# Optimization experiments

Measured on AMD Instinct MI355X. Metric: run time of the kernel, lower is better.

## Reference

```python
import jax, jax.numpy as jnp
import numpy as np

N_NODES = 100000
N_EDGES = 1000000
D_MODEL = 128
EDGE_DIM = 64
LN_EPS = 1e-5


def _layernorm(x, gamma, beta, eps=LN_EPS):
    mu = jnp.mean(x, axis=-1, keepdims=True)
    var = jnp.var(x, axis=-1, keepdims=True)
    return (x - mu) * jax.lax.rsqrt(var + eps) * gamma + beta


def setup_inputs() -> dict:
    key = jax.random.key(0)
    ks = jax.random.split(key, 12)
    std = 1.0 / np.sqrt(D_MODEL)
    stde = 1.0 / np.sqrt(EDGE_DIM)
    return {
        "x_src": jax.random.normal(ks[0], (N_NODES, D_MODEL), jnp.float32),
        "x_dst": jax.random.normal(ks[1], (N_NODES, D_MODEL), jnp.float32),
        "edge_attr": jax.random.normal(ks[2], (N_EDGES, EDGE_DIM), jnp.float32),
        "edge_index": jax.random.randint(ks[3], (2, N_EDGES), 0, N_NODES, jnp.int32),
        # params
        "W_src": jax.random.uniform(ks[4], (D_MODEL, D_MODEL), jnp.float32, -std, std),
        "W_dst": jax.random.uniform(ks[5], (D_MODEL, D_MODEL), jnp.float32, -std, std),
        "b_dst": jnp.zeros((D_MODEL,), jnp.float32),
        "Wg1": jax.random.uniform(ks[6], (EDGE_DIM, D_MODEL), jnp.float32, -stde, stde),
        "bg1": jnp.zeros((D_MODEL,), jnp.float32),
        "Wg2": jax.random.uniform(ks[7], (D_MODEL, 1), jnp.float32, -std, std),
        "bg2": jnp.zeros((1,), jnp.float32),
        "gamma": jnp.ones((D_MODEL,), jnp.float32),
        "beta": jnp.zeros((D_MODEL,), jnp.float32),
    }


def reference(x_src, x_dst, edge_attr, edge_index,
              W_src, W_dst, b_dst, Wg1, bg1, Wg2, bg2, gamma, beta):
    s, d = edge_index[0], edge_index[1]
    n = x_dst.shape[0]
    # gather + linear (no bias): [E, D]
    msg = x_src[s] @ W_src
    # edge gate MLP: Linear -> gelu -> Linear (no norm, eval so no dropout)
    h = jax.nn.gelu(edge_attr @ Wg1 + bg1, approximate=False)
    gate = jax.nn.sigmoid(h @ Wg2 + bg2)  # [E, 1]
    msg = msg * gate
    # scatter-add aggregate + mean by in-degree (clamped at 1)
    out = jax.ops.segment_sum(msg, d, num_segments=n)
    deg = jax.ops.segment_sum(jnp.ones((msg.shape[0],), msg.dtype), d, num_segments=n)
    out = out / jnp.clip(deg, 1.0)[:, None]
    # residual-like combine, layernorm, gelu
    out = _layernorm(out + x_dst @ W_dst + b_dst, gamma, beta)
    return jax.nn.gelu(out, approximate=False)
```

## Files before the change

kernel.cpp:

```cpp
#include <hip/hip_runtime.h>
#include <hip/hip_fp16.h>
#include <math.h>

#define N_NODES 100000
#define N_EDGES 1000000
#define D_MODEL 128
#define EDGE_DIM 64
#define SCHUNK 250
#define NSB 400

typedef short bf16x8 __attribute__((ext_vector_type(8)));
typedef float f32x4 __attribute__((ext_vector_type(4)));

__device__ __forceinline__ short f2bf(float f) {
    union { float f; unsigned u; } v; v.f = f;
    unsigned r = v.u + 0x7FFFu + ((v.u >> 16) & 1u);
    return (short)(r >> 16);
}
__device__ __forceinline__ float gelu_fast(float x) {
    float t = 0.7978845608028654f * x * (1.0f + 0.044715f * x * x);
    float e = __expf(2.0f * t);
    return x * (1.0f - __builtin_amdgcn_rcpf(e + 1.0f));
}
__device__ __forceinline__ float sigmoid_fast(float x) {
    return __builtin_amdgcn_rcpf(1.0f + __expf(-x));
}
__device__ __forceinline__ float bflo(unsigned v) { return __uint_as_float(v << 16); }
__device__ __forceinline__ float bfhi(unsigned v) { return __uint_as_float(v & 0xFFFF0000u); }

__global__ __launch_bounds__(256) void k_zero_int(int* __restrict__ p, int n) {
    int i = blockIdx.x * 256 + threadIdx.x;
    if (i < n) p[i] = 0;
}

__global__ __launch_bounds__(256) void k_prep(
    const float* __restrict__ Ws, const float* __restrict__ Wd,
    const float* __restrict__ Wg1, short* __restrict__ frag)
{
    int g = blockIdx.x * 256 + threadIdx.x;
    if (g >= 5120) return;
    const float* W; short* T; int q;
    if (g < 2048)      { W = Ws;  T = frag;         q = g; }
    else if (g < 4096) { W = Wd;  T = frag + 16384; q = g - 2048; }
    else               { W = Wg1; T = frag + 32768; q = g - 4096; }
    int ls = q & 63, nt = (q >> 6) & 7, kb = q >> 9;
    int col = nt * 16 + (ls & 15);
    int k0 = kb * 32 + (ls >> 4) * 8;
    bf16x8 v;
    #pragma unroll
    for (int e = 0; e < 8; ++e) v[e] = f2bf(W[(k0 + e) * D_MODEL + col]);
    *reinterpret_cast<bf16x8*>(T + (size_t)q * 8) = v;
}

__global__ __launch_bounds__(256, 2) void k_node_linear(
    const float* __restrict__ x_src, const float* __restrict__ x_dst,
    const short* __restrict__ WsrcF, const short* __restrict__ WdstF,
    const float* __restrict__ b_dst,
    short* __restrict__ ysrc, short* __restrict__ z_bf)
{
    __shared__ __align__(16) short Bf[4][8][64][8];
    const int tid = threadIdx.x;
    const int lane = tid & 63;
    const int wid = tid >> 6;
    const int l15 = lane & 15;
    const int lg = lane >> 4;
    const int mat = blockIdx.y;
    const float* __restrict__ X = mat ? x_dst : x_src;
    const short* __restrict__ WF = mat ? WdstF : WsrcF;
    const int row0 = blockIdx.x * 128 + wid * 32;

    float4 av[4][2][2];
    #pragma unroll
    for (int kb = 0; kb < 4; ++kb)
        #pragma unroll
        for (int st = 0; st < 2; ++st) {
            int r = min(row0 + st * 16 + l15, N_NODES - 1);
            const float* p = X + (size_t)r * D_MODEL + kb * 32 + lg * 8;
            av[kb][st][0] = *reinterpret_cast<const float4*>(p);
            av[kb][st][1] = *reinterpret_cast<const float4*>(p + 4);
        }
    #pragma unroll
    for (int i = 0; i < 8; ++i)
        reinterpret_cast<int4*>(Bf)[tid + i * 256] =
            reinterpret_cast<const int4*>(WF)[tid + i * 256];
    __syncthreads();

    bf16x8 a[4][2];
    #pragma unroll
    for (int kb = 0; kb < 4; ++kb)
        #pragma unroll
        for (int st = 0; st < 2; ++st) {
            float4 v0 = av[kb][st][0], v1 = av[kb][st][1];
            bf16x8 t;
            t[0] = f2bf(v0.x); t[1] = f2bf(v0.y); t[2] = f2bf(v0.z); t[3] = f2bf(v0.w);
            t[4] = f2bf(v1.x); t[5] = f2bf(v1.y); t[6] = f2bf(v1.z); t[7] = f2bf(v1.w);
            a[kb][st] = t;
        }

    f32x4 acc[2][8];
    #pragma unroll
    for (int st = 0; st < 2; ++st)
        #pragma unroll
        for (int nt = 0; nt < 8; ++nt) { f32x4 zz = {0.f,0.f,0.f,0.f}; acc[st][nt] = zz; }

    #pragma unroll
    for (int kb = 0; kb < 4; ++kb)
        #pragma unroll
        for (int nt = 0; nt < 8; ++nt) {
            bf16x8 b = *reinterpret_cast<const bf16x8*>(&Bf[kb][nt][lane][0]);
            acc[0][nt] = __builtin_amdgcn_mfma_f32_16x16x32_bf16(a[kb][0], b, acc[0][nt], 0, 0, 0);
            acc[1][nt] = __builtin_amdgcn_mfma_f32_16x16x32_bf16(a[kb][1], b, acc[1][nt], 0, 0, 0);
        }

    #pragma unroll
    for (int st = 0; st < 2; ++st) {
        int rowb = row0 + st * 16 + lg * 4;
        #pragma unroll
        for (int nt = 0; nt < 8; ++nt) {
            int col = nt * 16 + l15;
            float bias = mat ? b_dst[col] : 0.0f;
            #pragma unroll
            for (int r = 0; r < 4; ++r) {
                int row = rowb + r;
                if (row < N_NODES) {
                    float v = acc[st][nt][r];
                    if (mat) z_bf[(size_t)row * D_MODEL + col] = f2bf(v + bias);
                    else     ysrc[(size_t)row * D_MODEL + col] = f2bf(v);
                }
            }
        }
    }
}

__global__ __launch_bounds__(256, 4) void k_gate_fill(
    const float* __restrict__ ea, const short* __restrict__ Wg1F,
    const float* __restrict__ bg1, const float* __restrict__ Wg2,
    const float* __restrict__ bg2,
    const int* __restrict__ dstI, const int* __restrict__ srcI,
    int* __restrict__ cursor, int* __restrict__ sg_s,
    unsigned short* __restrict__ sg_g)
{
    __shared__ __align__(16) short Bf[2][8][64][8];
    const int tid = threadIdx.x;
    const int lane = tid & 63;
    const int wid = tid >> 6;
    const int l15 = lane & 15;
    const int lg = lane >> 4;
    const int e0 = blockIdx.x * 128 + wid * 32;

    float4 av[2][2][2];
    #pragma unroll
    for (int kb = 0; kb < 2; ++kb)
        #pragma unroll
        for (int st = 0; st < 2; ++st) {
            int r = min(e0 + st * 16 + l15, N_EDGES - 1);
            const float* p = ea + (size_t)r * EDGE_DIM + kb * 32 + lg * 8;
            av[kb][st][0] = *reinterpret_cast<const float4*>(p);
            av[kb][st][1] = *reinterpret_cast<const float4*>(p + 4);
        }
    float b1v[2][4], w2v[2][4];
    #pragma unroll
    for (int ntc = 0; ntc < 2; ++ntc)
        #pragma unroll
        for (int nt = 0; nt < 4; ++nt) {
            int col = (ntc * 4 + nt) * 16 + l15;
            b1v[ntc][nt] = bg1[col];
            w2v[ntc][nt] = Wg2[col];
        }
    #pragma unroll
    for (int i = 0; i < 4; ++i)
        reinterpret_cast<int4*>(Bf)[tid + i * 256] =
            reinterpret_cast<const int4*>(Wg1F)[tid + i * 256];
    __syncthreads();

    bf16x8 a[2][2];
    #pragma unroll
    for (int kb = 0; kb < 2; ++kb)
        #pragma unroll
        for (int st = 0; st < 2; ++st) {
            float4 v0 = av[kb][st][0], v1 = av[kb][st][1];
            bf16x8 t;
            t[0] = f2bf(v0.x); t[1] = f2bf(v0.y); t[2] = f2bf(v0.z); t[3] = f2bf(v0.w);
            t[4] = f2bf(v1.x); t[5] = f2bf(v1.y); t[6] = f2bf(v1.z); t[7] = f2bf(v1.w);
            a[kb][st] = t;
        }

    float part[2][4] = {{0.f,0.f,0.f,0.f},{0.f,0.f,0.f,0.f}};
    #pragma unroll
    for (int ntc = 0; ntc < 2; ++ntc) {
        f32x4 acc[2][4];
        #pragma unroll
        for (int st = 0; st < 2; ++st)
            #pragma unroll
            for (int nt = 0; nt < 4; ++nt) { f32x4 zz = {0.f,0.f,0.f,0.f}; acc[st][nt] = zz; }
        #pragma unroll
        for (int kb = 0; kb < 2; ++kb)
            #pragma unroll
            for (int nt = 0; nt < 4; ++nt) {
                bf16x8 b = *reinterpret_cast<const bf16x8*>(&Bf[kb][ntc * 4 + nt][lane][0]);
                acc[0][nt] = __builtin_amdgcn_mfma_f32_16x16x32_bf16(a[kb][0], b, acc[0][nt], 0, 0, 0);
                acc[1][nt] = __builtin_amdgcn_mfma_f32_16x16x32_bf16(a[kb][1], b, acc[1][nt], 0, 0, 0);
            }
        #pragma unroll
        for (int nt = 0; nt < 4; ++nt) {
            float b1 = b1v[ntc][nt], w2 = w2v[ntc][nt];
            #pragma unroll
            for (int st = 0; st < 2; ++st)
                #pragma unroll
                for (int r = 0; r < 4; ++r)
                    part[st][r] += gelu_fast(acc[st][nt][r] + b1) * w2;
        }
    }

    #pragma unroll
    for (int m = 1; m <= 8; m <<= 1)
        #pragma unroll
        for (int st = 0; st < 2; ++st)
            #pragma unroll
            for (int r = 0; r < 4; ++r)
                part[st][r] += __shfl_xor(part[st][r], m);

    if (l15 == 0) {
        float b2 = bg2[0];
        #pragma unroll
        for (int st = 0; st < 2; ++st)
            #pragma unroll
            for (int r = 0; r < 4; ++r) {
                int e = e0 + st * 16 + lg * 4 + r;
                if (e < N_EDGES) {
                    float gv = sigmoid_fast(part[st][r] + b2);
                    int d = dstI[e];
                    int s = srcI[e];
                    int p = atomicAdd(&cursor[d], 1);
                    __half h = __float2half(gv);
                    sg_s[p] = s;
                    sg_g[p] = *reinterpret_cast<unsigned short*>(&h);
                }
            }
    }
}

__global__ void k_deg(const int* __restrict__ dst, int* __restrict__ deg) {
    int e = blockIdx.x * 256 + threadIdx.x;
    if (e < N_EDGES) atomicAdd(&deg[dst[e]], 1);
}
__global__ __launch_bounds__(256) void k_scan1(const int* __restrict__ deg, int* __restrict__ bsum) {
    __shared__ int s[256];
    int tid = threadIdx.x;
    int i = blockIdx.x * SCHUNK + tid;
    int v = (tid < SCHUNK && i < N_NODES) ? deg[i] : 0;
    s[tid] = v; __syncthreads();
    for (int off = 128; off > 0; off >>= 1) {
        if (tid < off) s[tid] += s[tid + off];
        __syncthreads();
    }
    if (tid == 0) bsum[blockIdx.x] = s[0];
}
__global__ __launch_bounds__(512) void k_scan2(const int* __restrict__ bsum, int* __restrict__ boff) {
    __shared__ int s[512];
    int tid = threadIdx.x;
    int v = (tid < NSB) ? bsum[tid] : 0;
    s[tid] = v; __syncthreads();
    for (int off = 1; off < 512; off <<= 1) {
        int t = (tid >= off) ? s[tid - off] : 0;
        __syncthreads();
        s[tid] += t;
        __syncthreads();
    }
    if (tid < NSB) boff[tid] = s[tid] - v;
}
__global__ __launch_bounds__(256) void k_scan3(const int* __restrict__ deg, const int* __restrict__ boff,
                                               int* __restrict__ cursor) {
    __shared__ int s[256];
    int tid = threadIdx.x;
    int i = blockIdx.x * SCHUNK + tid;
    int v = (tid < SCHUNK && i < N_NODES) ? deg[i] : 0;
    s[tid] = v; __syncthreads();
    for (int off = 1; off < 256; off <<= 1) {
        int t = (tid >= off) ? s[tid - off] : 0;
        __syncthreads();
        s[tid] += t;
        __syncthreads();
    }
    int excl = s[tid] - v;
    if (tid < SCHUNK && i < N_NODES) cursor[i] = boff[blockIdx.x] + excl;
}

__global__ __launch_bounds__(256) void k_agg(
    const int* __restrict__ cursorEnd, const int* __restrict__ deg,
    const int* __restrict__ sg_s, const __half* __restrict__ sg_g,
    const short* __restrict__ ysrc, const short* __restrict__ z_bf,
    const float* __restrict__ gamma, const float* __restrict__ beta,
    float* __restrict__ out)
{
    const int lane = threadIdx.x & 63;
    const int wid = threadIdx.x >> 6;
    const int n = blockIdx.x * 4 + wid;
    const int dg = deg[n];
    const int start = cursorEnd[n] - dg;
    const int c0 = lane * 2;

    float a0 = 0.f, a1 = 0.f;
    int t = 0;
    for (; t + 4 <= dg; t += 4) {
        int s0 = sg_s[start + t + 0];
        int s1 = sg_s[start + t + 1];
        int s2 = sg_s[start + t + 2];
        int s3 = sg_s[start + t + 3];
        float g0 = __half2float(sg_g[start + t + 0]);
        float g1 = __half2float(sg_g[start + t + 1]);
        float g2 = __half2float(sg_g[start + t + 2]);
        float g3 = __half2float(sg_g[start + t + 3]);
        unsigned p0 = *reinterpret_cast<const unsigned*>(&ysrc[(size_t)s0 * D_MODEL + c0]);
        unsigned p1 = *reinterpret_cast<const unsigned*>(&ysrc[(size_t)s1 * D_MODEL + c0]);
        unsigned p2 = *reinterpret_cast<const unsigned*>(&ysrc[(size_t)s2 * D_MODEL + c0]);
        unsigned p3 = *reinterpret_cast<const unsigned*>(&ysrc[(size_t)s3 * D_MODEL + c0]);
        a0 += g0 * bflo(p0) + g1 * bflo(p1) + g2 * bflo(p2) + g3 * bflo(p3);
        a1 += g0 * bfhi(p0) + g1 * bfhi(p1) + g2 * bfhi(p2) + g3 * bfhi(p3);
    }
    for (; t < dg; ++t) {
        int s0 = sg_s[start + t];
        float g0 = __half2float(sg_g[start + t]);
        unsigned p0 = *reinterpret_cast<const unsigned*>(&ysrc[(size_t)s0 * D_MODEL + c0]);
        a0 += g0 * bflo(p0);
        a1 += g0 * bfhi(p0);
    }

    float inv = 1.0f / fmaxf((float)dg, 1.0f);
    unsigned zv = *reinterpret_cast<const unsigned*>(&z_bf[(size_t)n * D_MODEL + c0]);
    float t0 = a0 * inv + bflo(zv);
    float t1 = a1 * inv + bfhi(zv);

    float sum = t0 + t1;
    #pragma unroll
    for (int m = 1; m <= 32; m <<= 1) sum += __shfl_xor(sum, m);
    float mu = sum * (1.0f / 128.0f);
    float d0 = t0 - mu, d1 = t1 - mu;
    float vs = d0 * d0 + d1 * d1;
    #pragma unroll
    for (int m = 1; m <= 32; m <<= 1) vs += __shfl_xor(vs, m);
    float rstd = rsqrtf(vs * (1.0f / 128.0f) + 1e-5f);

    float2 gv = *reinterpret_cast<const float2*>(&gamma[c0]);
    float2 bv = *reinterpret_cast<const float2*>(&beta[c0]);
    float o0 = d0 * rstd * gv.x + bv.x;
    float o1 = d1 * rstd * gv.y + bv.y;
    float2 o = make_float2(gelu_fast(o0), gelu_fast(o1));
    *reinterpret_cast<float2*>(&out[(size_t)n * D_MODEL + c0]) = o;
}

extern "C" void kernel_launch(void* const* d_in, const int* in_sizes, int n_in,
                              void* d_out, int out_size, void* d_ws, size_t ws_size,
                              hipStream_t stream)
{
    const float* x_src = (const float*)d_in[0];
    const float* x_dst = (const float*)d_in[1];
    const float* ea    = (const float*)d_in[2];
    const int*   ei    = (const int*)d_in[3];
    const float* W_src = (const float*)d_in[4];
    const float* W_dst = (const float*)d_in[5];
    const float* b_dst = (const float*)d_in[6];
    const float* Wg1   = (const float*)d_in[7];
    const float* bg1   = (const float*)d_in[8];
    const float* Wg2   = (const float*)d_in[9];
    const float* bg2   = (const float*)d_in[10];
    const float* gamma = (const float*)d_in[11];
    const float* beta  = (const float*)d_in[12];
    const int* srcIdx = ei;
    const int* dstIdx = ei + N_EDGES;

    char* ws = (char*)d_ws;
    short*  fragT  = (short*)(ws);
    short*  ysrc   = (short*)(ws + 81920);
    short*  z_bf   = (short*)(ws + 25681920);
    int*    deg    = (int*)(ws + 51281920);
    int*    cursor = (int*)(ws + 51681920);
    int*    sg_s   = (int*)(ws + 52081920);
    unsigned short* sg_g = (unsigned short*)(ws + 56081920);
    int*    bsum   = (int*)(ws + 58081920);
    int*    boff   = (int*)(ws + 58083520);

    float* out = (float*)d_out;

    hipLaunchKernelGGL(k_zero_int, dim3((N_NODES + 255) / 256), dim3(256), 0, stream, deg, N_NODES);
    hipLaunchKernelGGL(k_deg, dim3(3907), dim3(256), 0, stream, dstIdx, deg);
    hipLaunchKernelGGL(k_scan1, dim3(NSB), dim3(256), 0, stream, deg, bsum);
    hipLaunchKernelGGL(k_scan2, dim3(1), dim3(512), 0, stream, bsum, boff);
    hipLaunchKernelGGL(k_scan3, dim3(NSB), dim3(256), 0, stream, deg, boff, cursor);
    hipLaunchKernelGGL(k_prep, dim3(20), dim3(256), 0, stream, W_src, W_dst, Wg1, fragT);
    hipLaunchKernelGGL(k_node_linear, dim3(782, 2), dim3(256), 0, stream,
                       x_src, x_dst, fragT, fragT + 16384, b_dst, ysrc, z_bf);
    hipLaunchKernelGGL(k_gate_fill, dim3(7813), dim3(256), 0, stream,
                       ea, fragT + 32768, bg1, Wg2, bg2, dstIdx, srcIdx, cursor, sg_s, sg_g);
    hipLaunchKernelGGL(k_agg, dim3(N_NODES / 4), dim3(256), 0, stream,
                       cursor, deg, sg_s, (const __half*)sg_g, ysrc, z_bf, gamma, beta, out);
}
```

Measured before the change: 293.5 us.

## Record per-edge rank in degree pass, pack CSR entries, fuse zeroing into prep

The degree-count atomic now returns each edge's rank, so the gate kernel computes its CSR slot directly from rstart[d] + rank[e] and no longer needs a second atomic on a cursor array. Source index and gate are packed into one int2 entry (the gate stays fp32 instead of fp16), so the aggregation reads a single 8-byte record per edge and gets its node range from rstart[n], rstart[n+1]. Degree zeroing is merged into the weight-prep kernel, removing one launch. Node-linear gains a double-buffered row load and a higher occupancy hint, and gate-fill loads its bias and weights inside the loop instead of holding them in registers. The cost is an extra 4 MB rank array that must be written and read back, plus larger CSR entries.

```diff
diff --git a/kernel.cpp b/kernel.cpp
--- a/kernel.cpp
+++ b/kernel.cpp
@@ -28,16 +28,18 @@
 __device__ __forceinline__ float bflo(unsigned v) { return __uint_as_float(v << 16); }
 __device__ __forceinline__ float bfhi(unsigned v) { return __uint_as_float(v & 0xFFFF0000u); }
 
-__global__ __launch_bounds__(256) void k_zero_int(int* __restrict__ p, int n) {
-    int i = blockIdx.x * 256 + threadIdx.x;
-    if (i < n) p[i] = 0;
-}
-
 __global__ __launch_bounds__(256) void k_prep(
     const float* __restrict__ Ws, const float* __restrict__ Wd,
-    const float* __restrict__ Wg1, short* __restrict__ frag)
+    const float* __restrict__ Wg1, short* __restrict__ frag,
+    int* __restrict__ deg)
 {
-    int g = blockIdx.x * 256 + threadIdx.x;
+    int b = blockIdx.x;
+    if (b >= 20) {
+        int i = (b - 20) * 256 + threadIdx.x;
+        if (i < N_NODES) deg[i] = 0;
+        return;
+    }
+    int g = b * 256 + threadIdx.x;
     if (g >= 5120) return;
     const float* W; short* T; int q;
     if (g < 2048)      { W = Ws;  T = frag;         q = g; }
@@ -52,7 +54,57 @@
     *reinterpret_cast<bf16x8*>(T + (size_t)q * 8) = v;
 }
 
-__global__ __launch_bounds__(256, 2) void k_node_linear(
+__global__ void k_deg(const int* __restrict__ dst, int* __restrict__ deg, int* __restrict__ rank) {
+    int e = blockIdx.x * 256 + threadIdx.x;
+    if (e < N_EDGES) rank[e] = atomicAdd(&deg[dst[e]], 1);
+}
+
+__global__ __launch_bounds__(256) void k_scan1(const int* __restrict__ deg, int* __restrict__ bsum) {
+    __shared__ int s[256];
+    int tid = threadIdx.x;
+    int i = blockIdx.x * SCHUNK + tid;
+    int v = (tid < SCHUNK && i < N_NODES) ? deg[i] : 0;
+    s[tid] = v; __syncthreads();
+    for (int off = 128; off > 0; off >>= 1) {
+        if (tid < off) s[tid] += s[tid + off];
+        __syncthreads();
+    }
+    if (tid == 0) bsum[blockIdx.x] = s[0];
+}
+__global__ __launch_bounds__(512) void k_scan2(const int* __restrict__ bsum, int* __restrict__ boff) {
+    __shared__ int s[512];
+    int tid = threadIdx.x;
+    int v = (tid < NSB) ? bsum[tid] : 0;
+    s[tid] = v; __syncthreads();
+    for (int off = 1; off < 512; off <<= 1) {
+        int t = (tid >= off) ? s[tid - off] : 0;
+        __syncthreads();
+        s[tid] += t;
+        __syncthreads();
+    }
+    if (tid < NSB) boff[tid] = s[tid] - v;
+}
+__global__ __launch_bounds__(256) void k_scan3(const int* __restrict__ deg, const int* __restrict__ boff,
+                                               int* __restrict__ rstart) {
+    __shared__ int s[256];
+    int tid = threadIdx.x;
+    int i = blockIdx.x * SCHUNK + tid;
+    int v = (tid < SCHUNK && i < N_NODES) ? deg[i] : 0;
+    s[tid] = v; __syncthreads();
+    for (int off = 1; off < 256; off <<= 1) {
+        int t = (tid >= off) ? s[tid - off] : 0;
+        __syncthreads();
+        s[tid] += t;
+        __syncthreads();
+    }
+    int excl = s[tid] - v;
+    if (tid < SCHUNK && i < N_NODES) {
+        rstart[i] = boff[blockIdx.x] + excl;
+        if (i == N_NODES - 1) rstart[N_NODES] = boff[blockIdx.x] + excl + v;
+    }
+}
+
+__global__ __launch_bounds__(256, 3) void k_node_linear(
     const float* __restrict__ x_src, const float* __restrict__ x_dst,
     const short* __restrict__ WsrcF, const short* __restrict__ WdstF,
     const float* __restrict__ b_dst,
@@ -69,48 +121,58 @@
     const short* __restrict__ WF = mat ? WdstF : WsrcF;
     const int row0 = blockIdx.x * 128 + wid * 32;
 
-    float4 av[4][2][2];
-    #pragma unroll
-    for (int kb = 0; kb < 4; ++kb)
-        #pragma unroll
-        for (int st = 0; st < 2; ++st) {
-            int r = min(row0 + st * 16 + l15, N_NODES - 1);
-            const float* p = X + (size_t)r * D_MODEL + kb * 32 + lg * 8;
-            av[kb][st][0] = *reinterpret_cast<const float4*>(p);
-            av[kb][st][1] = *reinterpret_cast<const float4*>(p + 4);
-        }
+    const float* rowp[2];
+    #pragma unroll
+    for (int st = 0; st < 2; ++st) {
+        int r = min(row0 + st * 16 + l15, N_NODES - 1);
+        rowp[st] = X + (size_t)r * D_MODEL + lg * 8;
+    }
+
+    float4 buf[2][2][2];
+    #pragma unroll
+    for (int st = 0; st < 2; ++st) {
+        buf[0][st][0] = *reinterpret_cast<const float4*>(rowp[st]);
+        buf[0][st][1] = *reinterpret_cast<const float4*>(rowp[st] + 4);
+    }
+
     #pragma unroll
     for (int i = 0; i < 8; ++i)
         reinterpret_cast<int4*>(Bf)[tid + i * 256] =
             reinterpret_cast<const int4*>(WF)[tid + i * 256];
+
+    f32x4 acc[2][8];
+    #pragma unroll
+    for (int st = 0; st < 2; ++st)
+        #pragma unroll
+        for (int nt = 0; nt < 8; ++nt) { f32x4 zz = {0.f,0.f,0.f,0.f}; acc[st][nt] = zz; }
+
     __syncthreads();
 
-    bf16x8 a[4][2];
-    #pragma unroll
-    for (int kb = 0; kb < 4; ++kb)
+    #pragma unroll
+    for (int kb = 0; kb < 4; ++kb) {
+        if (kb < 3) {
+            #pragma unroll
+            for (int st = 0; st < 2; ++st) {
+                buf[(kb + 1) & 1][st][0] = *reinterpret_cast<const float4*>(rowp[st] + (kb + 1) * 32);
+                buf[(kb + 1) & 1][st][1] = *reinterpret_cast<const float4*>(rowp[st] + (kb + 1) * 32 + 4);
+            }
+        }
+        bf16x8 a[2];
         #pragma unroll
         for (int st = 0; st < 2; ++st) {
-            float4 v0 = av[kb][st][0], v1 = av[kb][st][1];
+            float4 v0 = buf[kb & 1][st][0], v1 = buf[kb & 1][st][1];
             bf16x8 t;
             t[0] = f2bf(v0.x); t[1] = f2bf(v0.y); t[2] = f2bf(v0.z); t[3] = f2bf(v0.w);
             t[4] = f2bf(v1.x); t[5] = f2bf(v1.y); t[6] = f2bf(v1.z); t[7] = f2bf(v1.w);
-            a[kb][st] = t;
-        }
-
-    f32x4 acc[2][8];
-    #pragma unroll
-    for (int st = 0; st < 2; ++st)
-        #pragma unroll
-        for (int nt = 0; nt < 8; ++nt) { f32x4 zz = {0.f,0.f,0.f,0.f}; acc[st][nt] = zz; }
-
-    #pragma unroll
-    for (int kb = 0; kb < 4; ++kb)
+            a[st] = t;
+        }
         #pragma unroll
         for (int nt = 0; nt < 8; ++nt) {
             bf16x8 b = *reinterpret_cast<const bf16x8*>(&Bf[kb][nt][lane][0]);
-            acc[0][nt] = __builtin_amdgcn_mfma_f32_16x16x32_bf16(a[kb][0], b, acc[0][nt], 0, 0, 0);
-            acc[1][nt] = __builtin_amdgcn_mfma_f32_16x16x32_bf16(a[kb][1], b, acc[1][nt], 0, 0, 0);
-        }
+            acc[0][nt] = __builtin_amdgcn_mfma_f32_16x16x32_bf16(a[0], b, acc[0][nt], 0, 0, 0);
+            acc[1][nt] = __builtin_amdgcn_mfma_f32_16x16x32_bf16(a[1], b, acc[1][nt], 0, 0, 0);
+        }
+    }
 
     #pragma unroll
     for (int st = 0; st < 2; ++st) {
@@ -137,8 +199,8 @@
     const float* __restrict__ bg1, const float* __restrict__ Wg2,
     const float* __restrict__ bg2,
     const int* __restrict__ dstI, const int* __restrict__ srcI,
-    int* __restrict__ cursor, int* __restrict__ sg_s,
-    unsigned short* __restrict__ sg_g)
+    const int* __restrict__ rank, const int* __restrict__ rstart,
+    int2* __restrict__ sg)
 {
     __shared__ __align__(16) short Bf[2][8][64][8];
     const int tid = threadIdx.x;
@@ -158,15 +220,6 @@
             av[kb][st][0] = *reinterpret_cast<const float4*>(p);
             av[kb][st][1] = *reinterpret_cast<const float4*>(p + 4);
         }
-    float b1v[2][4], w2v[2][4];
-    #pragma unroll
-    for (int ntc = 0; ntc < 2; ++ntc)
-        #pragma unroll
-        for (int nt = 0; nt < 4; ++nt) {
-            int col = (ntc * 4 + nt) * 16 + l15;
-            b1v[ntc][nt] = bg1[col];
-            w2v[ntc][nt] = Wg2[col];
-        }
     #pragma unroll
     for (int i = 0; i < 4; ++i)
         reinterpret_cast<int4*>(Bf)[tid + i * 256] =
@@ -203,7 +256,9 @@
             }
         #pragma unroll
         for (int nt = 0; nt < 4; ++nt) {
-            float b1 = b1v[ntc][nt], w2 = w2v[ntc][nt];
+            int col = (ntc * 4 + nt) * 16 + l15;
+            float b1 = bg1[col];
+            float w2 = Wg2[col];
             #pragma unroll
             for (int st = 0; st < 2; ++st)
                 #pragma unroll
@@ -230,65 +285,16 @@
                 if (e < N_EDGES) {
                     float gv = sigmoid_fast(part[st][r] + b2);
                     int d = dstI[e];
-                    int s = srcI[e];
-                    int p = atomicAdd(&cursor[d], 1);
-                    __half h = __float2half(gv);
-                    sg_s[p] = s;
-                    sg_g[p] = *reinterpret_cast<unsigned short*>(&h);
+                    int p = rstart[d] + rank[e];
+                    int2 v; v.x = srcI[e]; v.y = __float_as_int(gv);
+                    sg[p] = v;
                 }
             }
     }
 }
 
-__global__ void k_deg(const int* __restrict__ dst, int* __restrict__ deg) {
-    int e = blockIdx.x * 256 + threadIdx.x;
-    if (e < N_EDGES) atomicAdd(&deg[dst[e]], 1);
-}
-__global__ __launch_bounds__(256) void k_scan1(const int* __restrict__ deg, int* __restrict__ bsum) {
-    __shared__ int s[256];
-    int tid = threadIdx.x;
-    int i = blockIdx.x * SCHUNK + tid;
-    int v = (tid < SCHUNK && i < N_NODES) ? deg[i] : 0;
-    s[tid] = v; __syncthreads();
-    for (int off = 128; off > 0; off >>= 1) {
-        if (tid < off) s[tid] += s[tid + off];
-        __syncthreads();
-    }
-    if (tid == 0) bsum[blockIdx.x] = s[0];
-}
-__global__ __launch_bounds__(512) void k_scan2(const int* __restrict__ bsum, int* __restrict__ boff) {
-    __shared__ int s[512];
-    int tid = threadIdx.x;
-    int v = (tid < NSB) ? bsum[tid] : 0;
-    s[tid] = v; __syncthreads();
-    for (int off = 1; off < 512; off <<= 1) {
-        int t = (tid >= off) ? s[tid - off] : 0;
-        __syncthreads();
-        s[tid] += t;
-        __syncthreads();
-    }
-    if (tid < NSB) boff[tid] = s[tid] - v;
-}
-__global__ __launch_bounds__(256) void k_scan3(const int* __restrict__ deg, const int* __restrict__ boff,
-                                               int* __restrict__ cursor) {
-    __shared__ int s[256];
-    int tid = threadIdx.x;
-    int i = blockIdx.x * SCHUNK + tid;
-    int v = (tid < SCHUNK && i < N_NODES) ? deg[i] : 0;
-    s[tid] = v; __syncthreads();
-    for (int off = 1; off < 256; off <<= 1) {
-        int t = (tid >= off) ? s[tid - off] : 0;
-        __syncthreads();
-        s[tid] += t;
-        __syncthreads();
-    }
-    int excl = s[tid] - v;
-    if (tid < SCHUNK && i < N_NODES) cursor[i] = boff[blockIdx.x] + excl;
-}
-
 __global__ __launch_bounds__(256) void k_agg(
-    const int* __restrict__ cursorEnd, const int* __restrict__ deg,
-    const int* __restrict__ sg_s, const __half* __restrict__ sg_g,
+    const int* __restrict__ rstart, const int2* __restrict__ sg,
     const short* __restrict__ ysrc, const short* __restrict__ z_bf,
     const float* __restrict__ gamma, const float* __restrict__ beta,
     float* __restrict__ out)
@@ -296,38 +302,40 @@
     const int lane = threadIdx.x & 63;
     const int wid = threadIdx.x >> 6;
     const int n = blockIdx.x * 4 + wid;
-    const int dg = deg[n];
-    const int start = cursorEnd[n] - dg;
+    const int start = rstart[n];
+    const int end = rstart[n + 1];
+    const int dg = end - start;
     const int c0 = lane * 2;
 
+    unsigned zv = *reinterpret_cast<const unsigned*>(&z_bf[(size_t)n * D_MODEL + c0]);
+    float2 gv = *reinterpret_cast<const float2*>(&gamma[c0]);
+    float2 bv = *reinterpret_cast<const float2*>(&beta[c0]);
+
     float a0 = 0.f, a1 = 0.f;
-    int t = 0;
-    for (; t + 4 <= dg; t += 4) {
-        int s0 = sg_s[start + t + 0];
-        int s1 = sg_s[start + t + 1];
-        int s2 = sg_s[start + t + 2];
-        int s3 = sg_s[start + t + 3];
-        float g0 = __half2float(sg_g[start + t + 0]);
-        float g1 = __half2float(sg_g[start + t + 1]);
-        float g2 = __half2float(sg_g[start + t + 2]);
-        float g3 = __half2float(sg_g[start + t + 3]);
-        unsigned p0 = *reinterpret_cast<const unsigned*>(&ysrc[(size_t)s0 * D_MODEL + c0]);
-        unsigned p1 = *reinterpret_cast<const unsigned*>(&ysrc[(size_t)s1 * D_MODEL + c0]);
-        unsigned p2 = *reinterpret_cast<const unsigned*>(&ysrc[(size_t)s2 * D_MODEL + c0]);
-        unsigned p3 = *reinterpret_cast<const unsigned*>(&ysrc[(size_t)s3 * D_MODEL + c0]);
+    int t = start;
+    for (; t + 4 <= end; t += 4) {
+        int2 e0 = sg[t + 0];
+        int2 e1 = sg[t + 1];
+        int2 e2 = sg[t + 2];
+        int2 e3 = sg[t + 3];
+        unsigned p0 = *reinterpret_cast<const unsigned*>(&ysrc[(size_t)e0.x * D_MODEL + c0]);
+        unsigned p1 = *reinterpret_cast<const unsigned*>(&ysrc[(size_t)e1.x * D_MODEL + c0]);
+        unsigned p2 = *reinterpret_cast<const unsigned*>(&ysrc[(size_t)e2.x * D_MODEL + c0]);
+        unsigned p3 = *reinterpret_cast<const unsigned*>(&ysrc[(size_t)e3.x * D_MODEL + c0]);
+        float g0 = __int_as_float(e0.y), g1 = __int_as_float(e1.y);
+        float g2 = __int_as_float(e2.y), g3 = __int_as_float(e3.y);
         a0 += g0 * bflo(p0) + g1 * bflo(p1) + g2 * bflo(p2) + g3 * bflo(p3);
         a1 += g0 * bfhi(p0) + g1 * bfhi(p1) + g2 * bfhi(p2) + g3 * bfhi(p3);
     }
-    for (; t < dg; ++t) {
-        int s0 = sg_s[start + t];
-        float g0 = __half2float(sg_g[start + t]);
-        unsigned p0 = *reinterpret_cast<const unsigned*>(&ysrc[(size_t)s0 * D_MODEL + c0]);
+    for (; t < end; ++t) {
+        int2 e0 = sg[t];
+        float g0 = __int_as_float(e0.y);
+        unsigned p0 = *reinterpret_cast<const unsigned*>(&ysrc[(size_t)e0.x * D_MODEL + c0]);
         a0 += g0 * bflo(p0);
         a1 += g0 * bfhi(p0);
     }
 
     float inv = 1.0f / fmaxf((float)dg, 1.0f);
-    unsigned zv = *reinterpret_cast<const unsigned*>(&z_bf[(size_t)n * D_MODEL + c0]);
     float t0 = a0 * inv + bflo(zv);
     float t1 = a1 * inv + bfhi(zv);
 
@@ -341,8 +349,6 @@
     for (int m = 1; m <= 32; m <<= 1) vs += __shfl_xor(vs, m);
     float rstd = rsqrtf(vs * (1.0f / 128.0f) + 1e-5f);
 
-    float2 gv = *reinterpret_cast<const float2*>(&gamma[c0]);
-    float2 bv = *reinterpret_cast<const float2*>(&beta[c0]);
     float o0 = d0 * rstd * gv.x + bv.x;
     float o1 = d1 * rstd * gv.y + bv.y;
     float2 o = make_float2(gelu_fast(o0), gelu_fast(o1));
@@ -370,28 +376,27 @@
     const int* dstIdx = ei + N_EDGES;
 
     char* ws = (char*)d_ws;
-    short*  fragT  = (short*)(ws);
-    short*  ysrc   = (short*)(ws + 81920);
-    short*  z_bf   = (short*)(ws + 25681920);
-    int*    deg    = (int*)(ws + 51281920);
-    int*    cursor = (int*)(ws + 51681920);
-    int*    sg_s   = (int*)(ws + 52081920);
-    unsigned short* sg_g = (unsigned short*)(ws + 56081920);
-    int*    bsum   = (int*)(ws + 58081920);
-    int*    boff   = (int*)(ws + 58083520);
+    short* fragT  = (short*)(ws);
+    short* ysrc   = (short*)(ws + 81920);
+    short* z_bf   = (short*)(ws + 25681920);
+    int*   deg    = (int*)(ws + 51281920);
+    int*   rank   = (int*)(ws + 51681920);
+    int*   rstart = (int*)(ws + 55681920);
+    int2*  sg     = (int2*)(ws + 56082336);
+    int*   bsum   = (int*)(ws + 64082336);
+    int*   boff   = (int*)(ws + 64084000);
 
     float* out = (float*)d_out;
 
-    hipLaunchKernelGGL(k_zero_int, dim3((N_NODES + 255) / 256), dim3(256), 0, stream, deg, N_NODES);
-    hipLaunchKernelGGL(k_deg, dim3(3907), dim3(256), 0, stream, dstIdx, deg);
+    hipLaunchKernelGGL(k_prep, dim3(411), dim3(256), 0, stream, W_src, W_dst, Wg1, fragT, deg);
+    hipLaunchKernelGGL(k_deg, dim3(3907), dim3(256), 0, stream, dstIdx, deg, rank);
     hipLaunchKernelGGL(k_scan1, dim3(NSB), dim3(256), 0, stream, deg, bsum);
     hipLaunchKernelGGL(k_scan2, dim3(1), dim3(512), 0, stream, bsum, boff);
-    hipLaunchKernelGGL(k_scan3, dim3(NSB), dim3(256), 0, stream, deg, boff, cursor);
-    hipLaunchKernelGGL(k_prep, dim3(20), dim3(256), 0, stream, W_src, W_dst, Wg1, fragT);
+    hipLaunchKernelGGL(k_scan3, dim3(NSB), dim3(256), 0, stream, deg, boff, rstart);
     hipLaunchKernelGGL(k_node_linear, dim3(782, 2), dim3(256), 0, stream,
                        x_src, x_dst, fragT, fragT + 16384, b_dst, ysrc, z_bf);
     hipLaunchKernelGGL(k_gate_fill, dim3(7813), dim3(256), 0, stream,
-                       ea, fragT + 32768, bg1, Wg2, bg2, dstIdx, srcIdx, cursor, sg_s, sg_g);
+                       ea, fragT + 32768, bg1, Wg2, bg2, dstIdx, srcIdx, rank, rstart, sg);
     hipLaunchKernelGGL(k_agg, dim3(N_NODES / 4), dim3(256), 0, stream,
-                       cursor, deg, sg_s, (const __half*)sg_g, ysrc, z_bf, gamma, beta, out);
-}
+                       rstart, sg, ysrc, z_bf, gamma, beta, out);
+}
```

After: 277.8 us. 1.06x faster.
